# Kernel optimization log

Hardware: AMD Instinct MI355X
Metric: run time of the kernel (lower is better)

## Reference

```python
import jax, jax.numpy as jnp
import numpy as np

B = 32; D = 192; DEPTH = 4; DI = 384; DS = 16; DC = 4; P = 16; IMG = 224; N = 196; NC = 2


def setup_inputs() -> dict:
    key = jax.random.key(0)
    ks = iter(jax.random.split(key, 20))
    rn = lambda shape, s=0.02: jax.random.normal(next(ks), shape, dtype=jnp.float32) * s
    inp = {}
    inp["x"] = jax.random.normal(next(ks), (B, 3, IMG, IMG), dtype=jnp.float32)
    inp["patch_w"] = rn((D, 3 * P * P)); inp["patch_b"] = jnp.zeros((D,), jnp.float32)
    inp["cls_token"] = rn((1, 1, D)); inp["pos_embed"] = rn((1, N + 1, D))
    inp["ln_g"] = jnp.ones((DEPTH, D), jnp.float32); inp["ln_b"] = jnp.zeros((DEPTH, D), jnp.float32)
    inp["w_in"] = rn((DEPTH, 2 * DI, D))
    inp["conv_w"] = rn((DEPTH, DI, DC)); inp["conv_b"] = jnp.zeros((DEPTH, DI), jnp.float32)
    inp["w_x"] = rn((DEPTH, 2 * DS + 1, DI))
    inp["w_dt"] = rn((DEPTH, DI)); inp["b_dt"] = jnp.zeros((DEPTH, DI), jnp.float32)
    A = jnp.tile(jnp.arange(1, DS + 1, dtype=jnp.float32)[None, None, :], (DEPTH, DI, 1))
    inp["A_log"] = jnp.log(A)
    inp["D_ssm"] = jnp.ones((DEPTH, DI), jnp.float32)
    inp["w_out"] = rn((DEPTH, D, DI))
    inp["fn_g"] = jnp.ones((D,), jnp.float32); inp["fn_b"] = jnp.zeros((D,), jnp.float32)
    inp["cls_w"] = rn((NC, D)); inp["cls_b"] = jnp.zeros((NC,), jnp.float32)
    inp["reg_w1"] = rn((D // 2, D)); inp["reg_b1"] = jnp.zeros((D // 2,), jnp.float32)
    inp["reg_w2"] = rn((1, D // 2)); inp["reg_b2"] = jnp.zeros((1,), jnp.float32)
    return inp


def _ln(x, g, b):
    m = x.mean(-1, keepdims=True)
    v = ((x - m) ** 2).mean(-1, keepdims=True)
    return (x - m) / jnp.sqrt(v + 1e-5) * g + b


def _mamba(x, w_in, conv_w, conv_b, w_x, w_dt, b_dt, A_log, D_ssm, w_out):
    Bb, L, _ = x.shape
    xz = jnp.einsum('bld,ed->ble', x, w_in)           # [B,L,2*DI]
    xc, z = xz[..., :DI], xz[..., DI:]
    # causal depthwise conv1d (torch pads both sides then slices [:L] -> left-pad DC-1)
    xct = jnp.transpose(xc, (0, 2, 1))                 # [B,DI,L]
    xpad = jnp.pad(xct, ((0, 0), (0, 0), (DC - 1, 0)))
    conv = sum(conv_w[:, k, None] * xpad[:, :, k:k + L] for k in range(DC)) + conv_b[:, None]
    xa = jax.nn.silu(jnp.transpose(conv, (0, 2, 1)))   # [B,L,DI]
    bcd = jnp.einsum('bld,nd->bln', xa, w_x)           # [B,L,2*DS+1]
    Bm = bcd[..., :DS]; Cm = bcd[..., DS:2 * DS]
    dt = jax.nn.softplus(bcd[..., -1:] * w_dt + b_dt)  # [B,L,DI]  (Linear(1,DI))
    A = -jnp.exp(A_log)                                # [DI,DS]
    dA = jnp.exp(dt[..., None] * A)                    # [B,L,DI,DS]
    dBx = dt[..., None] * Bm[:, :, None, :] * xa[..., None]

    def step(h, inp):
        dA_t, dBx_t, C_t = inp
        h = dA_t * h + dBx_t
        return h, jnp.einsum('bdn,bn->bd', h, C_t)

    h0 = jnp.zeros((Bb, DI, DS), dtype=x.dtype)
    _, ys = jax.lax.scan(step, h0, (dA.transpose(1, 0, 2, 3), dBx.transpose(1, 0, 2, 3), Cm.transpose(1, 0, 2)))
    y = jnp.transpose(ys, (1, 0, 2)) + xa * D_ssm
    return jnp.einsum('bli,di->bld', y * jax.nn.silu(z), w_out)


def reference(x, patch_w, patch_b, cls_token, pos_embed, ln_g, ln_b, w_in, conv_w, conv_b,
              w_x, w_dt, b_dt, A_log, D_ssm, w_out, fn_g, fn_b, cls_w, cls_b,
              reg_w1, reg_b1, reg_w2, reg_b2):
    Bb = x.shape[0]
    H = IMG // P
    # non-overlapping patchify == Conv2d(kernel=stride=P)
    patches = x.reshape(Bb, 3, H, P, H, P).transpose(0, 2, 4, 1, 3, 5).reshape(Bb, N, 3 * P * P)
    tok = patches @ patch_w.T + patch_b
    t = jnp.concatenate([jnp.broadcast_to(cls_token, (Bb, 1, D)), tok], axis=1) + pos_embed
    for i in range(DEPTH):
        t = t + _mamba(_ln(t, ln_g[i], ln_b[i]), w_in[i], conv_w[i], conv_b[i],
                       w_x[i], w_dt[i], b_dt[i], A_log[i], D_ssm[i], w_out[i])
    feat = _ln(t, fn_g, fn_b)[:, 0]
    cls = feat @ cls_w.T + cls_b
    reg = jax.nn.gelu(feat @ reg_w1.T + reg_b1, approximate=False) @ reg_w2.T + reg_b2
    return (cls, reg)
```

## Files before the change

### kernel.cpp

```cpp
#include <hip/hip_runtime.h>
#include <hip/hip_bf16.h>
#include <math.h>

#define B_ 32
#define D_ 192
#define DEPTH_ 4
#define DI_ 384
#define DS_ 16
#define DC_ 4
#define P_ 16
#define IMG_ 224
#define N_ 196
#define L_ 197

#define NCH 16
#define CHL 13

typedef short s16x8 __attribute__((ext_vector_type(8)));
typedef float f32x16 __attribute__((ext_vector_type(16)));

__device__ __forceinline__ float sigmoidf_(float x) { return 1.f / (1.f + expf(-x)); }

__global__ __launch_bounds__(256) void k_prep(const float* __restrict__ patch_w,
                                              const float* __restrict__ w_in,
                                              const float* __restrict__ w_out,
                                              const float* __restrict__ w_x,
                                              const float* __restrict__ cls_tok,
                                              const float* __restrict__ pos,
                                              const float* __restrict__ A_log,
                                              __hip_bfloat16* __restrict__ pw,
                                              __hip_bfloat16* __restrict__ win,
                                              __hip_bfloat16* __restrict__ wout,
                                              __hip_bfloat16* __restrict__ wx,
                                              float* __restrict__ t,
                                              float* __restrict__ Aneg) {
  int idx = blockIdx.x * 256 + threadIdx.x;
  if (idx < 147456) { pw[idx] = __float2bfloat16(patch_w[idx]); return; }
  idx -= 147456;
  if (idx < 589824) { win[idx] = __float2bfloat16(w_in[idx]); return; }
  idx -= 589824;
  if (idx < 294912) { wout[idx] = __float2bfloat16(w_out[idx]); return; }
  idx -= 294912;
  if (idx < 98304) {
    int li = idx / 24576;
    int r = (idx / 384) & 63;
    int c = idx % 384;
    wx[idx] = (r < 33) ? __float2bfloat16(w_x[(li * 33 + r) * 384 + c]) : __float2bfloat16(0.f);
    return;
  }
  idx -= 98304;
  if (idx < 6144) {
    int b = idx / 192, d = idx % 192;
    t[(size_t)b * L_ * D_ + d] = cls_tok[d] + pos[d];
    return;
  }
  idx -= 6144;
  Aneg[idx] = -expf(A_log[idx]);
}

__global__ __launch_bounds__(256) void k_im2col(const float* __restrict__ x,
                                                __hip_bfloat16* __restrict__ A) {
  int idx = blockIdx.x * 256 + threadIdx.x;
  int tok = idx / 768, f = idx - tok * 768;
  int b = tok / 196, p = tok - b * 196;
  int h = p / 14, w = p - h * 14;
  int c = f >> 8, i = (f >> 4) & 15, j = f & 15;
  float v = x[(((size_t)(b * 3 + c) * 224 + h * 16 + i) * 224 + w * 16 + j)];
  A[idx] = __float2bfloat16(v);
}

template <int KTOT, int MODE>
__global__ __launch_bounds__(256) void k_gemm_mfma(const short* __restrict__ A,
                                                   const short* __restrict__ Wb,
                                                   float* __restrict__ C,
                                                   const float* __restrict__ bias,
                                                   const float* __restrict__ pos,
                                                   int M) {
  constexpr int KC = 96;
  constexpr int STR = 104;
  __shared__ __align__(16) short Als[64 * STR];
  __shared__ __align__(16) short Bls[64 * STR];
  int m0 = blockIdx.x * 64, n0 = blockIdx.y * 64;
  int tid = threadIdx.x;
  int lane = tid & 63, wid = tid >> 6;
  int mw = (wid & 1) * 32, nw = (wid >> 1) * 32;
  int l31 = lane & 31, lh = lane >> 5;
  f32x16 acc;
#pragma unroll
  for (int i = 0; i < 16; i++) acc[i] = 0.f;
  for (int kc = 0; kc < KTOT; kc += KC) {
    __syncthreads();
#pragma unroll
    for (int i = 0; i < 3; i++) {
      int seg = tid + i * 256;
      int r = seg / 12, s = seg - r * 12;
      *(s16x8*)(Als + r * STR + s * 8) =
          *(const s16x8*)(A + (size_t)(m0 + r) * KTOT + kc + s * 8);
      *(s16x8*)(Bls + r * STR + s * 8) =
          *(const s16x8*)(Wb + (size_t)(n0 + r) * KTOT + kc + s * 8);
    }
    __syncthreads();
#pragma unroll
    for (int ks = 0; ks < KC / 16; ks++) {
      s16x8 af = *(const s16x8*)(Als + (mw + l31) * STR + ks * 16 + lh * 8);
      s16x8 bf = *(const s16x8*)(Bls + (nw + l31) * STR + ks * 16 + lh * 8);
      acc = __builtin_amdgcn_mfma_f32_32x32x16_bf16(af, bf, acc, 0, 0, 0);
    }
  }
  int gn = n0 + nw + l31;
#pragma unroll
  for (int i = 0; i < 16; i++) {
    int rowt = mw + (i & 3) + 8 * (i >> 2) + 4 * lh;
    int gm = m0 + rowt;
    float v = acc[i];
    if (MODE == 1) {
      if (gm < M) C[(size_t)gm * 192 + gn] += v;
    } else if (MODE == 3) {
      if (gm < M) C[(size_t)gm * 64 + gn] = v;
    } else if (MODE == 4) {
      if (gm < M) ((__hip_bfloat16*)C)[(size_t)gm * 768 + gn] = __float2bfloat16(v);
    } else {
      int b = gm / 196, p = gm - b * 196;
      C[((size_t)b * 197 + 1 + p) * 192 + gn] =
          v + bias[gn] + pos[(size_t)(1 + p) * 192 + gn];
    }
  }
}

__global__ __launch_bounds__(256) void k_ln_bf(const float* __restrict__ t,
                                               const float* __restrict__ g,
                                               const float* __restrict__ bb,
                                               __hip_bfloat16* __restrict__ o) {
  int tok = blockIdx.x * 4 + (threadIdx.x >> 6);
  int tid = threadIdx.x & 63;
  const float* xr = t + (size_t)tok * D_;
  float x0 = xr[tid], x1 = xr[tid + 64], x2 = xr[tid + 128];
  float s = x0 + x1 + x2;
  float q = x0 * x0 + x1 * x1 + x2 * x2;
#pragma unroll
  for (int off = 1; off < 64; off <<= 1) {
    s += __shfl_xor(s, off, 64);
    q += __shfl_xor(q, off, 64);
  }
  float m = s * (1.f / 192.f);
  float r = rsqrtf(q * (1.f / 192.f) - m * m + 1e-5f);
  __hip_bfloat16* orow = o + (size_t)tok * D_;
  orow[tid]       = __float2bfloat16((x0 - m) * r * g[tid]       + bb[tid]);
  orow[tid + 64]  = __float2bfloat16((x1 - m) * r * g[tid + 64]  + bb[tid + 64]);
  orow[tid + 128] = __float2bfloat16((x2 - m) * r * g[tid + 128] + bb[tid + 128]);
}

__global__ __launch_bounds__(384) void k_conv(const __hip_bfloat16* __restrict__ xz,
                                              const float* __restrict__ cw_,
                                              const float* __restrict__ cb,
                                              __hip_bfloat16* __restrict__ xa_bf,
                                              __hip_bfloat16* __restrict__ sz_bf) {
  __shared__ float xs[11][384];
  int r0 = blockIdx.x * 8;
  int d = threadIdx.x;
#pragma unroll
  for (int row = 0; row < 11; row++) {
    int gr = r0 - 3 + row;
    if (gr >= 0) xs[row][d] = __bfloat162float(xz[(size_t)gr * 768 + d]);
  }
  __syncthreads();
  float4 cw = *(const float4*)(cw_ + d * 4);
  float cbv = cb[d];
#pragma unroll
  for (int tk = 0; tk < 8; tk++) {
    int tok = r0 + tk;
    int l = tok % L_;
    float acc = fmaf(cw.w, xs[tk + 3][d], cbv);
    if (l >= 1) acc = fmaf(cw.z, xs[tk + 2][d], acc);
    if (l >= 2) acc = fmaf(cw.y, xs[tk + 1][d], acc);
    if (l >= 3) acc = fmaf(cw.x, xs[tk][d], acc);
    float xav = acc * sigmoidf_(acc);
    xa_bf[(size_t)tok * DI_ + d] = __float2bfloat16(xav);
    float z = __bfloat162float(xz[(size_t)tok * 768 + 384 + d]);
    sz_bf[(size_t)tok * DI_ + d] = __float2bfloat16(z * sigmoidf_(z));
  }
}

__global__ __launch_bounds__(384) void k_scan1(const __hip_bfloat16* __restrict__ xa,
                                               const float* __restrict__ bcd,
                                               const float* __restrict__ Aneg,
                                               const float* __restrict__ w_dt,
                                               const float* __restrict__ b_dt,
                                               float* __restrict__ Pst,
                                               float* __restrict__ Hst) {
  int b = blockIdx.x >> 4, ch = blockIdx.x & 15;
  int d = threadIdx.x;
  int l0 = ch * CHL;
  int lim = min(CHL, L_ - l0);
  float Av[16];
#pragma unroll
  for (int q = 0; q < 4; q++) {
    float4 v = *(const float4*)(Aneg + d * 16 + q * 4);
    Av[q * 4] = v.x; Av[q * 4 + 1] = v.y; Av[q * 4 + 2] = v.z; Av[q * 4 + 3] = v.w;
  }
  float wdt = w_dt[d], bdt = b_dt[d];
  const __hip_bfloat16* xap = xa + ((size_t)b * L_ + l0) * DI_ + d;
  const float* bp = bcd + ((size_t)b * L_ + l0) * 64;
  float h[16], Pp[16];
#pragma unroll
  for (int n = 0; n < 16; n++) { h[n] = 0.f; Pp[n] = 1.f; }
  float xv = __bfloat162float(xap[0]);
  for (int j = 0; j < lim; j++) {
    int jn = (j + 1 < lim) ? (j + 1) : j;
    float xn = __bfloat162float(xap[(size_t)jn * DI_]);
    float dtraw = bp[j * 64 + 32];
    float Bn[16];
#pragma unroll
    for (int n = 0; n < 16; n++) Bn[n] = bp[j * 64 + n];
    float v = fmaf(dtraw, wdt, bdt);
    float dtv = (v > 20.f) ? v : __logf(1.f + __expf(v));
    float dtx = dtv * xv;
#pragma unroll
    for (int n = 0; n < 16; n++) {
      float dA = __expf(dtv * Av[n]);
      h[n] = fmaf(dA, h[n], dtx * Bn[n]);
      Pp[n] *= dA;
    }
    xv = xn;
  }
  size_t s = ((size_t)blockIdx.x * 384 + d) * 16;
#pragma unroll
  for (int q = 0; q < 4; q++) {
    *(float4*)(Pst + s + q * 4) = make_float4(Pp[q * 4], Pp[q * 4 + 1], Pp[q * 4 + 2], Pp[q * 4 + 3]);
    *(float4*)(Hst + s + q * 4) = make_float4(h[q * 4], h[q * 4 + 1], h[q * 4 + 2], h[q * 4 + 3]);
  }
}

__global__ __launch_bounds__(256) void k_scan_mid(const float* __restrict__ Pst,
                                                  const float* __restrict__ Hst,
                                                  float* __restrict__ Hinit) {
  int idx = blockIdx.x * 256 + threadIdx.x;
  int b = idx / 6144, r = idx - b * 6144;
  float h = 0.f;
#pragma unroll
  for (int c = 0; c < NCH; c++) {
    size_t o = (size_t)(b * NCH + c) * 6144 + r;
    Hinit[o] = h;
    h = fmaf(Pst[o], h, Hst[o]);
  }
}

__global__ __launch_bounds__(384) void k_scan2(const __hip_bfloat16* __restrict__ xa,
                                               const __hip_bfloat16* __restrict__ sz,
                                               const float* __restrict__ bcd,
                                               const float* __restrict__ Aneg,
                                               const float* __restrict__ D_ssm,
                                               const float* __restrict__ w_dt,
                                               const float* __restrict__ b_dt,
                                               const float* __restrict__ Hinit,
                                               __hip_bfloat16* __restrict__ y) {
  int b = blockIdx.x >> 4, ch = blockIdx.x & 15;
  int d = threadIdx.x;
  int l0 = ch * CHL;
  int lim = min(CHL, L_ - l0);
  float Av[16];
#pragma unroll
  for (int q = 0; q < 4; q++) {
    float4 v = *(const float4*)(Aneg + d * 16 + q * 4);
    Av[q * 4] = v.x; Av[q * 4 + 1] = v.y; Av[q * 4 + 2] = v.z; Av[q * 4 + 3] = v.w;
  }
  float Dv = D_ssm[d];
  float wdt = w_dt[d], bdt = b_dt[d];
  const __hip_bfloat16* xap = xa + ((size_t)b * L_ + l0) * DI_ + d;
  const __hip_bfloat16* szp = sz + ((size_t)b * L_ + l0) * DI_ + d;
  const float* bp = bcd + ((size_t)b * L_ + l0) * 64;
  __hip_bfloat16* yp = y + ((size_t)b * L_ + l0) * DI_ + d;
  float h[16];
  {
    size_t s = ((size_t)blockIdx.x * 384 + d) * 16;
#pragma unroll
    for (int q = 0; q < 4; q++) {
      float4 v = *(const float4*)(Hinit + s + q * 4);
      h[q * 4] = v.x; h[q * 4 + 1] = v.y; h[q * 4 + 2] = v.z; h[q * 4 + 3] = v.w;
    }
  }
  float xv = __bfloat162float(xap[0]);
  float szv = __bfloat162float(szp[0]);
  for (int j = 0; j < lim; j++) {
    int jn = (j + 1 < lim) ? (j + 1) : j;
    float xn = __bfloat162float(xap[(size_t)jn * DI_]);
    float szn = __bfloat162float(szp[(size_t)jn * DI_]);
    float dtraw = bp[j * 64 + 32];
    float Bn[16], Cn[16];
#pragma unroll
    for (int n = 0; n < 16; n++) Bn[n] = bp[j * 64 + n];
#pragma unroll
    for (int n = 0; n < 16; n++) Cn[n] = bp[j * 64 + 16 + n];
    float v = fmaf(dtraw, wdt, bdt);
    float dtv = (v > 20.f) ? v : __logf(1.f + __expf(v));
    float dtx = dtv * xv;
    float acc = 0.f;
#pragma unroll
    for (int n = 0; n < 16; n++) {
      float dA = __expf(dtv * Av[n]);
      h[n] = fmaf(dA, h[n], dtx * Bn[n]);
      acc = fmaf(h[n], Cn[n], acc);
    }
    float yv = fmaf(xv, Dv, acc) * szv;
    yp[(size_t)j * DI_] = __float2bfloat16(yv);
    xv = xn; szv = szn;
  }
}

__global__ __launch_bounds__(192) void k_head(const float* __restrict__ t,
                                              const float* __restrict__ fn_g,
                                              const float* __restrict__ fn_b,
                                              const float* __restrict__ cls_w,
                                              const float* __restrict__ cls_b,
                                              const float* __restrict__ rw1,
                                              const float* __restrict__ rb1,
                                              const float* __restrict__ rw2,
                                              const float* __restrict__ rb2,
                                              float* __restrict__ out) {
  __shared__ float red[8];
  __shared__ float stats[2];
  __shared__ float feat_s[192];
  __shared__ float h_s[96];
  int b = blockIdx.x, tid = threadIdx.x;
  float x = t[(size_t)b * L_ * D_ + tid];
  float s = x, q = x * x;
#pragma unroll
  for (int off = 1; off < 64; off <<= 1) {
    s += __shfl_xor(s, off, 64);
    q += __shfl_xor(q, off, 64);
  }
  int w = tid >> 6;
  if ((tid & 63) == 0) { red[w] = s; red[4 + w] = q; }
  __syncthreads();
  if (tid == 0) {
    float ss = red[0] + red[1] + red[2];
    float qq = red[4] + red[5] + red[6];
    float m = ss * (1.f / 192.f);
    stats[0] = m;
    stats[1] = rsqrtf(qq * (1.f / 192.f) - m * m + 1e-5f);
  }
  __syncthreads();
  float fv = (x - stats[0]) * stats[1] * fn_g[tid] + fn_b[tid];
  feat_s[tid] = fv;
  __syncthreads();
  if (tid < 96) {
    float a = rb1[tid];
    const float* wr = rw1 + (size_t)tid * 192;
    for (int k = 0; k < 192; k++) a = fmaf(feat_s[k], wr[k], a);
    h_s[tid] = 0.5f * a * (1.f + erff(a * 0.70710678118654752f));
  } else if (tid < 98) {
    int c = tid - 96;
    float a = cls_b[c];
    const float* wr = cls_w + (size_t)c * 192;
    for (int k = 0; k < 192; k++) a = fmaf(feat_s[k], wr[k], a);
    out[b * 2 + c] = a;
  }
  __syncthreads();
  if (tid == 0) {
    float a = rb2[0];
    for (int j = 0; j < 96; j++) a = fmaf(h_s[j], rw2[j], a);
    out[64 + b] = a;
  }
}

extern "C" void kernel_launch(void* const* d_in, const int* in_sizes, int n_in,
                              void* d_out, int out_size, void* d_ws, size_t ws_size,
                              hipStream_t stream) {
  const float* x       = (const float*)d_in[0];
  const float* patch_w = (const float*)d_in[1];
  const float* patch_b = (const float*)d_in[2];
  const float* cls_tok = (const float*)d_in[3];
  const float* pos     = (const float*)d_in[4];
  const float* ln_g    = (const float*)d_in[5];
  const float* ln_b    = (const float*)d_in[6];
  const float* w_in    = (const float*)d_in[7];
  const float* conv_w  = (const float*)d_in[8];
  const float* conv_b  = (const float*)d_in[9];
  const float* w_x     = (const float*)d_in[10];
  const float* w_dt    = (const float*)d_in[11];
  const float* b_dt    = (const float*)d_in[12];
  const float* A_log   = (const float*)d_in[13];
  const float* D_ssm   = (const float*)d_in[14];
  const float* w_out   = (const float*)d_in[15];
  const float* fn_g    = (const float*)d_in[16];
  const float* fn_b    = (const float*)d_in[17];
  const float* cls_w   = (const float*)d_in[18];
  const float* cls_b   = (const float*)d_in[19];
  const float* reg_w1  = (const float*)d_in[20];
  const float* reg_b1  = (const float*)d_in[21];
  const float* reg_w2  = (const float*)d_in[22];
  const float* reg_b2  = (const float*)d_in[23];
  float* out = (float*)d_out;

  float* ws = (float*)d_ws;
  float* t_buf = ws;
  float* bcd   = t_buf + 1210368;
  float* Pst   = bcd + 405504;
  float* Hst   = Pst + 3145728;
  float* Hinit = Hst + 3145728;
  float* Aneg  = Hinit + 3145728;
  __hip_bfloat16* xz_bf  = (__hip_bfloat16*)(Aneg + 24576);
  __hip_bfloat16* Abuf   = xz_bf;
  __hip_bfloat16* xa_bf  = xz_bf + 4841472;
  __hip_bfloat16* sz_bf  = xa_bf + 2433024;
  __hip_bfloat16* xln_bf = sz_bf + 2433024;
  __hip_bfloat16* y_bf   = xln_bf + 1216512;
  __hip_bfloat16* pw_bf  = y_bf + 2433024;
  __hip_bfloat16* win_bf = pw_bf + 147456;
  __hip_bfloat16* wout_bf = win_bf + 589824;
  __hip_bfloat16* wx_bf  = wout_bf + 294912;

  k_prep<<<4536, 256, 0, stream>>>(patch_w, w_in, w_out, w_x, cls_tok, pos, A_log,
                                   pw_bf, win_bf, wout_bf, wx_bf, t_buf, Aneg);
  k_im2col<<<18816, 256, 0, stream>>>(x, Abuf);
  k_gemm_mfma<768, 2><<<dim3(98, 3), 256, 0, stream>>>(
      (const short*)Abuf, (const short*)pw_bf, t_buf, patch_b, pos, 6272);

  for (int i = 0; i < DEPTH_; i++) {
    k_ln_bf<<<1576, 256, 0, stream>>>(t_buf, ln_g + i * D_, ln_b + i * D_, xln_bf);
    k_gemm_mfma<192, 4><<<dim3(99, 12), 256, 0, stream>>>(
        (const short*)xln_bf, (const short*)(win_bf + (size_t)i * 147456), (float*)xz_bf,
        nullptr, nullptr, 6304);
    k_conv<<<788, 384, 0, stream>>>(xz_bf, conv_w + i * DI_ * DC_, conv_b + i * DI_,
                                    xa_bf, sz_bf);
    k_gemm_mfma<384, 3><<<dim3(99, 1), 256, 0, stream>>>(
        (const short*)xa_bf, (const short*)(wx_bf + (size_t)i * 24576), bcd,
        nullptr, nullptr, 6304);
    k_scan1<<<B_ * NCH, 384, 0, stream>>>(xa_bf, bcd, Aneg + i * 6144,
                                          w_dt + i * DI_, b_dt + i * DI_, Pst, Hst);
    k_scan_mid<<<768, 256, 0, stream>>>(Pst, Hst, Hinit);
    k_scan2<<<B_ * NCH, 384, 0, stream>>>(xa_bf, sz_bf, bcd, Aneg + i * 6144,
                                          D_ssm + i * DI_, w_dt + i * DI_, b_dt + i * DI_,
                                          Hinit, y_bf);
    k_gemm_mfma<384, 1><<<dim3(99, 3), 256, 0, stream>>>(
        (const short*)y_bf, (const short*)(wout_bf + (size_t)i * 73728), t_buf,
        nullptr, nullptr, 6304);
  }
  k_head<<<32, 192, 0, stream>>>(t_buf, fn_g, fn_b, cls_w, cls_b, reg_w1, reg_b1,
                                 reg_w2, reg_b2, out);
}
```

Before: 462.0 us.

## Fuse LayerNorm into GEMM epilogues, conv into x_proj GEMM, inline scan combine

Merges im2col with weight prep. The patch GEMM and the out-projection GEMM now use full-row 64x192 tiles, so each can add the residual and compute the next layer's LayerNorm in its epilogue. The depthwise conv plus SiLU now feeds the B/C/dt projection GEMM through shared memory, and the z-gate SiLU is computed in the same kernel. The separate scan_mid kernel is removed: each scan2 block recomputes its chunk-initial state from the per-chunk P/H summaries. This cuts launches and global round-trips, but the full-row GEMMs run only 99 blocks, which lowers parallelism, and later scan chunks repeat the prefix work.

```diff
diff --git a/kernel.cpp b/kernel.cpp
--- a/kernel.cpp
+++ b/kernel.cpp
@@ -20,21 +20,35 @@
 typedef float f32x16 __attribute__((ext_vector_type(16)));
 
 __device__ __forceinline__ float sigmoidf_(float x) { return 1.f / (1.f + expf(-x)); }
-
-__global__ __launch_bounds__(256) void k_prep(const float* __restrict__ patch_w,
-                                              const float* __restrict__ w_in,
-                                              const float* __restrict__ w_out,
-                                              const float* __restrict__ w_x,
-                                              const float* __restrict__ cls_tok,
-                                              const float* __restrict__ pos,
-                                              const float* __restrict__ A_log,
-                                              __hip_bfloat16* __restrict__ pw,
-                                              __hip_bfloat16* __restrict__ win,
-                                              __hip_bfloat16* __restrict__ wout,
-                                              __hip_bfloat16* __restrict__ wx,
-                                              float* __restrict__ t,
-                                              float* __restrict__ Aneg) {
-  int idx = blockIdx.x * 256 + threadIdx.x;
+__device__ __forceinline__ float bf2f(short s) {
+  unsigned int u = ((unsigned int)(unsigned short)s) << 16;
+  return __uint_as_float(u);
+}
+__device__ __forceinline__ short f2bf(float f) {
+  __hip_bfloat16 h = __float2bfloat16(f);
+  return *(short*)&h;
+}
+
+__global__ __launch_bounds__(256) void k_prep_im2col(
+    const float* __restrict__ x, __hip_bfloat16* __restrict__ A,
+    const float* __restrict__ patch_w, const float* __restrict__ w_in,
+    const float* __restrict__ w_out, const float* __restrict__ w_x,
+    const float* __restrict__ cls_tok, const float* __restrict__ pos,
+    const float* __restrict__ A_log,
+    __hip_bfloat16* __restrict__ pw, __hip_bfloat16* __restrict__ win,
+    __hip_bfloat16* __restrict__ wout, __hip_bfloat16* __restrict__ wx,
+    float* __restrict__ t, float* __restrict__ Aneg) {
+  if (blockIdx.x < 18816) {
+    int idx = blockIdx.x * 256 + threadIdx.x;
+    int tok = idx / 768, f = idx - tok * 768;
+    int b = tok / 196, p = tok - b * 196;
+    int h = p / 14, w = p - h * 14;
+    int c = f >> 8, i = (f >> 4) & 15, j = f & 15;
+    float v = x[(((size_t)(b * 3 + c) * 224 + h * 16 + i) * 224 + w * 16 + j)];
+    A[idx] = __float2bfloat16(v);
+    return;
+  }
+  int idx = (blockIdx.x - 18816) * 256 + threadIdx.x;
   if (idx < 147456) { pw[idx] = __float2bfloat16(patch_w[idx]); return; }
   idx -= 147456;
   if (idx < 589824) { win[idx] = __float2bfloat16(w_in[idx]); return; }
@@ -58,25 +72,104 @@
   Aneg[idx] = -expf(A_log[idx]);
 }
 
-__global__ __launch_bounds__(256) void k_im2col(const float* __restrict__ x,
-                                                __hip_bfloat16* __restrict__ A) {
-  int idx = blockIdx.x * 256 + threadIdx.x;
-  int tok = idx / 768, f = idx - tok * 768;
-  int b = tok / 196, p = tok - b * 196;
-  int h = p / 14, w = p - h * 14;
-  int c = f >> 8, i = (f >> 4) & 15, j = f & 15;
-  float v = x[(((size_t)(b * 3 + c) * 224 + h * 16 + i) * 224 + w * 16 + j)];
-  A[idx] = __float2bfloat16(v);
-}
-
-template <int KTOT, int MODE>
-__global__ __launch_bounds__(256) void k_gemm_mfma(const short* __restrict__ A,
-                                                   const short* __restrict__ Wb,
-                                                   float* __restrict__ C,
-                                                   const float* __restrict__ bias,
-                                                   const float* __restrict__ pos,
-                                                   int M) {
-  constexpr int KC = 96;
+__global__ __launch_bounds__(256) void k_patch_ln(const short* __restrict__ A,
+                                                  const short* __restrict__ pw,
+                                                  const float* __restrict__ pb,
+                                                  const float* __restrict__ pos,
+                                                  float* __restrict__ t,
+                                                  const float* __restrict__ g,
+                                                  const float* __restrict__ bb,
+                                                  __hip_bfloat16* __restrict__ xln) {
+  __shared__ __align__(16) char smem[53248];
+  short* Als = (short*)smem;
+  short* Bls = Als + 64 * 104;
+  float* ts = (float*)smem;
+  int m0 = blockIdx.x * 64;
+  int tid = threadIdx.x;
+  int lane = tid & 63, wid = tid >> 6;
+  int mw = (wid & 1) * 32, nw = (wid >> 1) * 96;
+  int l31 = lane & 31, lh = lane >> 5;
+  f32x16 acc[3];
+#pragma unroll
+  for (int j = 0; j < 3; j++)
+#pragma unroll
+    for (int i = 0; i < 16; i++) acc[j][i] = 0.f;
+  for (int kc = 0; kc < 768; kc += 96) {
+    __syncthreads();
+#pragma unroll
+    for (int i = 0; i < 3; i++) {
+      int seg = tid + i * 256;
+      int r = seg / 12, s = seg - r * 12;
+      int tok = m0 + r;
+      int b = tok / 197, l = tok - b * 197;
+      s16x8 v = {0, 0, 0, 0, 0, 0, 0, 0};
+      if (tok < 6304 && l > 0)
+        v = *(const s16x8*)(A + ((size_t)(b * 196 + l - 1)) * 768 + kc + s * 8);
+      *(s16x8*)(Als + r * 104 + s * 8) = v;
+    }
+#pragma unroll
+    for (int i = 0; i < 9; i++) {
+      int seg = tid + i * 256;
+      int r = seg / 12, s = seg - r * 12;
+      *(s16x8*)(Bls + r * 104 + s * 8) = *(const s16x8*)(pw + (size_t)r * 768 + kc + s * 8);
+    }
+    __syncthreads();
+#pragma unroll
+    for (int ks = 0; ks < 6; ks++) {
+      s16x8 af = *(const s16x8*)(Als + (mw + l31) * 104 + ks * 16 + lh * 8);
+#pragma unroll
+      for (int j = 0; j < 3; j++) {
+        s16x8 bf = *(const s16x8*)(Bls + (nw + j * 32 + l31) * 104 + ks * 16 + lh * 8);
+        acc[j] = __builtin_amdgcn_mfma_f32_32x32x16_bf16(af, bf, acc[j], 0, 0, 0);
+      }
+    }
+  }
+  __syncthreads();
+#pragma unroll
+  for (int j = 0; j < 3; j++) {
+    int gnl = nw + j * 32 + l31;
+#pragma unroll
+    for (int i = 0; i < 16; i++) {
+      int rowt = mw + (i & 3) + 8 * (i >> 2) + 4 * lh;
+      ts[rowt * 193 + gnl] = acc[j][i];
+    }
+  }
+  __syncthreads();
+  int r = tid >> 2, part = tid & 3;
+  int tok = m0 + r;
+  int l = tok % 197;
+  bool valid = tok < 6304;
+  float* trow = t + (size_t)tok * 192;
+  float s = 0.f, q = 0.f;
+  for (int jj = 0; jj < 48; jj++) {
+    int col = part * 48 + jj;
+    float v;
+    if (l == 0) {
+      v = valid ? trow[col] : 0.f;
+    } else {
+      v = ts[r * 193 + col] + pb[col] + pos[(size_t)l * 192 + col];
+      if (valid) trow[col] = v;
+    }
+    ts[r * 193 + col] = v;
+    s += v; q += v * v;
+  }
+  s += __shfl_xor(s, 1, 4); s += __shfl_xor(s, 2, 4);
+  q += __shfl_xor(q, 1, 4); q += __shfl_xor(q, 2, 4);
+  float m = s * (1.f / 192.f);
+  float rinv = rsqrtf(q * (1.f / 192.f) - m * m + 1e-5f);
+  if (valid) {
+    __hip_bfloat16* xrow = xln + (size_t)tok * 192;
+    for (int jj = 0; jj < 48; jj++) {
+      int col = part * 48 + jj;
+      float v = ts[r * 193 + col];
+      xrow[col] = __float2bfloat16((v - m) * rinv * g[col] + bb[col]);
+    }
+  }
+}
+
+__global__ __launch_bounds__(256) void k_gemm_in(const short* __restrict__ A,
+                                                 const short* __restrict__ Wb,
+                                                 __hip_bfloat16* __restrict__ C) {
   constexpr int STR = 104;
   __shared__ __align__(16) short Als[64 * STR];
   __shared__ __align__(16) short Bls[64 * STR];
@@ -88,20 +181,20 @@
   f32x16 acc;
 #pragma unroll
   for (int i = 0; i < 16; i++) acc[i] = 0.f;
-  for (int kc = 0; kc < KTOT; kc += KC) {
+  for (int kc = 0; kc < 192; kc += 96) {
     __syncthreads();
 #pragma unroll
     for (int i = 0; i < 3; i++) {
       int seg = tid + i * 256;
       int r = seg / 12, s = seg - r * 12;
       *(s16x8*)(Als + r * STR + s * 8) =
-          *(const s16x8*)(A + (size_t)(m0 + r) * KTOT + kc + s * 8);
+          *(const s16x8*)(A + (size_t)(m0 + r) * 192 + kc + s * 8);
       *(s16x8*)(Bls + r * STR + s * 8) =
-          *(const s16x8*)(Wb + (size_t)(n0 + r) * KTOT + kc + s * 8);
-    }
-    __syncthreads();
-#pragma unroll
-    for (int ks = 0; ks < KC / 16; ks++) {
+          *(const s16x8*)(Wb + (size_t)(n0 + r) * 192 + kc + s * 8);
+    }
+    __syncthreads();
+#pragma unroll
+    for (int ks = 0; ks < 6; ks++) {
       s16x8 af = *(const s16x8*)(Als + (mw + l31) * STR + ks * 16 + lh * 8);
       s16x8 bf = *(const s16x8*)(Bls + (nw + l31) * STR + ks * 16 + lh * 8);
       acc = __builtin_amdgcn_mfma_f32_32x32x16_bf16(af, bf, acc, 0, 0, 0);
@@ -112,72 +205,104 @@
   for (int i = 0; i < 16; i++) {
     int rowt = mw + (i & 3) + 8 * (i >> 2) + 4 * lh;
     int gm = m0 + rowt;
-    float v = acc[i];
-    if (MODE == 1) {
-      if (gm < M) C[(size_t)gm * 192 + gn] += v;
-    } else if (MODE == 3) {
-      if (gm < M) C[(size_t)gm * 64 + gn] = v;
-    } else if (MODE == 4) {
-      if (gm < M) ((__hip_bfloat16*)C)[(size_t)gm * 768 + gn] = __float2bfloat16(v);
-    } else {
-      int b = gm / 196, p = gm - b * 196;
-      C[((size_t)b * 197 + 1 + p) * 192 + gn] =
-          v + bias[gn] + pos[(size_t)(1 + p) * 192 + gn];
-    }
-  }
-}
-
-__global__ __launch_bounds__(256) void k_ln_bf(const float* __restrict__ t,
-                                               const float* __restrict__ g,
-                                               const float* __restrict__ bb,
-                                               __hip_bfloat16* __restrict__ o) {
-  int tok = blockIdx.x * 4 + (threadIdx.x >> 6);
-  int tid = threadIdx.x & 63;
-  const float* xr = t + (size_t)tok * D_;
-  float x0 = xr[tid], x1 = xr[tid + 64], x2 = xr[tid + 128];
-  float s = x0 + x1 + x2;
-  float q = x0 * x0 + x1 * x1 + x2 * x2;
-#pragma unroll
-  for (int off = 1; off < 64; off <<= 1) {
-    s += __shfl_xor(s, off, 64);
-    q += __shfl_xor(q, off, 64);
-  }
-  float m = s * (1.f / 192.f);
-  float r = rsqrtf(q * (1.f / 192.f) - m * m + 1e-5f);
-  __hip_bfloat16* orow = o + (size_t)tok * D_;
-  orow[tid]       = __float2bfloat16((x0 - m) * r * g[tid]       + bb[tid]);
-  orow[tid + 64]  = __float2bfloat16((x1 - m) * r * g[tid + 64]  + bb[tid + 64]);
-  orow[tid + 128] = __float2bfloat16((x2 - m) * r * g[tid + 128] + bb[tid + 128]);
-}
-
-__global__ __launch_bounds__(384) void k_conv(const __hip_bfloat16* __restrict__ xz,
-                                              const float* __restrict__ cw_,
-                                              const float* __restrict__ cb,
-                                              __hip_bfloat16* __restrict__ xa_bf,
-                                              __hip_bfloat16* __restrict__ sz_bf) {
-  __shared__ float xs[11][384];
-  int r0 = blockIdx.x * 8;
-  int d = threadIdx.x;
-#pragma unroll
-  for (int row = 0; row < 11; row++) {
-    int gr = r0 - 3 + row;
-    if (gr >= 0) xs[row][d] = __bfloat162float(xz[(size_t)gr * 768 + d]);
-  }
-  __syncthreads();
-  float4 cw = *(const float4*)(cw_ + d * 4);
-  float cbv = cb[d];
-#pragma unroll
-  for (int tk = 0; tk < 8; tk++) {
-    int tok = r0 + tk;
-    int l = tok % L_;
-    float acc = fmaf(cw.w, xs[tk + 3][d], cbv);
-    if (l >= 1) acc = fmaf(cw.z, xs[tk + 2][d], acc);
-    if (l >= 2) acc = fmaf(cw.y, xs[tk + 1][d], acc);
-    if (l >= 3) acc = fmaf(cw.x, xs[tk][d], acc);
-    float xav = acc * sigmoidf_(acc);
-    xa_bf[(size_t)tok * DI_ + d] = __float2bfloat16(xav);
-    float z = __bfloat162float(xz[(size_t)tok * 768 + 384 + d]);
-    sz_bf[(size_t)tok * DI_ + d] = __float2bfloat16(z * sigmoidf_(z));
+    if (gm < 6304) C[(size_t)gm * 768 + gn] = __float2bfloat16(acc[i]);
+  }
+}
+
+__global__ __launch_bounds__(256) void k_convbcd(const __hip_bfloat16* __restrict__ xz,
+                                                 const float* __restrict__ cw_,
+                                                 const float* __restrict__ cb_,
+                                                 const short* __restrict__ wx,
+                                                 float* __restrict__ bcd,
+                                                 __hip_bfloat16* __restrict__ xa_bf,
+                                                 __hip_bfloat16* __restrict__ sz_bf) {
+  __shared__ float xs[67 * 96];
+  __shared__ __align__(16) short Als[64 * 104];
+  __shared__ __align__(16) short Bls[64 * 104];
+  __shared__ float cws[96 * 4];
+  __shared__ float cbs[96];
+  int m0 = blockIdx.x * 64;
+  int tid = threadIdx.x;
+  int lane = tid & 63, wid = tid >> 6;
+  int mw = (wid & 1) * 32, nw = (wid >> 1) * 32;
+  int l31 = lane & 31, lh = lane >> 5;
+  f32x16 acc;
+#pragma unroll
+  for (int i = 0; i < 16; i++) acc[i] = 0.f;
+  for (int kc = 0; kc < 384; kc += 96) {
+    __syncthreads();
+#pragma unroll
+    for (int i = 0; i < 4; i++) {
+      int seg = tid + i * 256;
+      if (seg < 804) {
+        int row = seg / 12, s = seg - row * 12;
+        int tokp = m0 - 3 + row;
+        s16x8 v = {0, 0, 0, 0, 0, 0, 0, 0};
+        if (tokp >= 0 && tokp < 6304)
+          v = *(const s16x8*)((const short*)xz + (size_t)tokp * 768 + kc + s * 8);
+        float4 f0 = make_float4(bf2f(v[0]), bf2f(v[1]), bf2f(v[2]), bf2f(v[3]));
+        float4 f1 = make_float4(bf2f(v[4]), bf2f(v[5]), bf2f(v[6]), bf2f(v[7]));
+        *(float4*)(xs + row * 96 + s * 8) = f0;
+        *(float4*)(xs + row * 96 + s * 8 + 4) = f1;
+      }
+    }
+    if (tid < 96) {
+      *(float4*)(cws + tid * 4) = *(const float4*)(cw_ + (kc + tid) * 4);
+      cbs[tid] = cb_[kc + tid];
+    }
+#pragma unroll
+    for (int i = 0; i < 3; i++) {
+      int seg = tid + i * 256;
+      int r = seg / 12, s = seg - r * 12;
+      *(s16x8*)(Bls + r * 104 + s * 8) = *(const s16x8*)(wx + (size_t)r * 384 + kc + s * 8);
+    }
+    __syncthreads();
+#pragma unroll
+    for (int i = 0; i < 24; i++) {
+      int idx = tid + i * 256;
+      int orow = idx / 96, c = idx - orow * 96;
+      int tok = m0 + orow;
+      int l = tok % 197;
+      float4 cw = *(const float4*)(cws + c * 4);
+      float a = fmaf(cw.w, xs[(orow + 3) * 96 + c], cbs[c]);
+      if (l >= 1) a = fmaf(cw.z, xs[(orow + 2) * 96 + c], a);
+      if (l >= 2) a = fmaf(cw.y, xs[(orow + 1) * 96 + c], a);
+      if (l >= 3) a = fmaf(cw.x, xs[orow * 96 + c], a);
+      float xav = a * sigmoidf_(a);
+      short bv = f2bf(xav);
+      Als[orow * 104 + c] = bv;
+      if (tok < 6304) ((short*)xa_bf)[(size_t)tok * 384 + kc + c] = bv;
+    }
+    __syncthreads();
+#pragma unroll
+    for (int ks = 0; ks < 6; ks++) {
+      s16x8 af = *(const s16x8*)(Als + (mw + l31) * 104 + ks * 16 + lh * 8);
+      s16x8 bf = *(const s16x8*)(Bls + (nw + l31) * 104 + ks * 16 + lh * 8);
+      acc = __builtin_amdgcn_mfma_f32_32x32x16_bf16(af, bf, acc, 0, 0, 0);
+    }
+  }
+  int gn = nw + l31;
+#pragma unroll
+  for (int i = 0; i < 16; i++) {
+    int rowt = mw + (i & 3) + 8 * (i >> 2) + 4 * lh;
+    int gm = m0 + rowt;
+    if (gm < 6304) bcd[(size_t)gm * 64 + gn] = acc[i];
+  }
+#pragma unroll
+  for (int i = 0; i < 12; i++) {
+    int seg = tid + i * 256;
+    int r = seg / 48, s = seg - r * 48;
+    int tok = m0 + r;
+    if (tok < 6304) {
+      s16x8 zv = *(const s16x8*)((const short*)xz + (size_t)tok * 768 + 384 + s * 8);
+      s16x8 ov;
+#pragma unroll
+      for (int e = 0; e < 8; e++) {
+        float z = bf2f(zv[e]);
+        ov[e] = f2bf(z * sigmoidf_(z));
+      }
+      *(s16x8*)((short*)sz_bf + (size_t)tok * 384 + s * 8) = ov;
+    }
   }
 }
 
@@ -231,20 +356,6 @@
   }
 }
 
-__global__ __launch_bounds__(256) void k_scan_mid(const float* __restrict__ Pst,
-                                                  const float* __restrict__ Hst,
-                                                  float* __restrict__ Hinit) {
-  int idx = blockIdx.x * 256 + threadIdx.x;
-  int b = idx / 6144, r = idx - b * 6144;
-  float h = 0.f;
-#pragma unroll
-  for (int c = 0; c < NCH; c++) {
-    size_t o = (size_t)(b * NCH + c) * 6144 + r;
-    Hinit[o] = h;
-    h = fmaf(Pst[o], h, Hst[o]);
-  }
-}
-
 __global__ __launch_bounds__(384) void k_scan2(const __hip_bfloat16* __restrict__ xa,
                                                const __hip_bfloat16* __restrict__ sz,
                                                const float* __restrict__ bcd,
@@ -252,7 +363,8 @@
                                                const float* __restrict__ D_ssm,
                                                const float* __restrict__ w_dt,
                                                const float* __restrict__ b_dt,
-                                               const float* __restrict__ Hinit,
+                                               const float* __restrict__ Pst,
+                                               const float* __restrict__ Hst,
                                                __hip_bfloat16* __restrict__ y) {
   int b = blockIdx.x >> 4, ch = blockIdx.x & 15;
   int d = threadIdx.x;
@@ -266,19 +378,25 @@
   }
   float Dv = D_ssm[d];
   float wdt = w_dt[d], bdt = b_dt[d];
+  float h[16];
+#pragma unroll
+  for (int n = 0; n < 16; n++) h[n] = 0.f;
+  for (int c = 0; c < ch; c++) {
+    size_t o = ((size_t)(b * NCH + c) * 384 + d) * 16;
+#pragma unroll
+    for (int q = 0; q < 4; q++) {
+      float4 P = *(const float4*)(Pst + o + q * 4);
+      float4 H = *(const float4*)(Hst + o + q * 4);
+      h[q * 4]     = fmaf(P.x, h[q * 4],     H.x);
+      h[q * 4 + 1] = fmaf(P.y, h[q * 4 + 1], H.y);
+      h[q * 4 + 2] = fmaf(P.z, h[q * 4 + 2], H.z);
+      h[q * 4 + 3] = fmaf(P.w, h[q * 4 + 3], H.w);
+    }
+  }
   const __hip_bfloat16* xap = xa + ((size_t)b * L_ + l0) * DI_ + d;
   const __hip_bfloat16* szp = sz + ((size_t)b * L_ + l0) * DI_ + d;
   const float* bp = bcd + ((size_t)b * L_ + l0) * 64;
   __hip_bfloat16* yp = y + ((size_t)b * L_ + l0) * DI_ + d;
-  float h[16];
-  {
-    size_t s = ((size_t)blockIdx.x * 384 + d) * 16;
-#pragma unroll
-    for (int q = 0; q < 4; q++) {
-      float4 v = *(const float4*)(Hinit + s + q * 4);
-      h[q * 4] = v.x; h[q * 4 + 1] = v.y; h[q * 4 + 2] = v.z; h[q * 4 + 3] = v.w;
-    }
-  }
   float xv = __bfloat162float(xap[0]);
   float szv = __bfloat162float(szp[0]);
   for (int j = 0; j < lim; j++) {
@@ -304,6 +422,95 @@
     float yv = fmaf(xv, Dv, acc) * szv;
     yp[(size_t)j * DI_] = __float2bfloat16(yv);
     xv = xn; szv = szn;
+  }
+}
+
+template <bool DO_LN>
+__global__ __launch_bounds__(256) void k_out_ln(const short* __restrict__ A,
+                                                const short* __restrict__ wout,
+                                                float* __restrict__ t,
+                                                const float* __restrict__ g,
+                                                const float* __restrict__ bb,
+                                                __hip_bfloat16* __restrict__ xln) {
+  __shared__ __align__(16) char smem[53248];
+  short* Als = (short*)smem;
+  short* Bls = Als + 64 * 104;
+  float* ts = (float*)smem;
+  int m0 = blockIdx.x * 64;
+  int tid = threadIdx.x;
+  int lane = tid & 63, wid = tid >> 6;
+  int mw = (wid & 1) * 32, nw = (wid >> 1) * 96;
+  int l31 = lane & 31, lh = lane >> 5;
+  f32x16 acc[3];
+#pragma unroll
+  for (int j = 0; j < 3; j++)
+#pragma unroll
+    for (int i = 0; i < 16; i++) acc[j][i] = 0.f;
+  for (int kc = 0; kc < 384; kc += 96) {
+    __syncthreads();
+#pragma unroll
+    for (int i = 0; i < 3; i++) {
+      int seg = tid + i * 256;
+      int r = seg / 12, s = seg - r * 12;
+      *(s16x8*)(Als + r * 104 + s * 8) =
+          *(const s16x8*)(A + (size_t)(m0 + r) * 384 + kc + s * 8);
+    }
+#pragma unroll
+    for (int i = 0; i < 9; i++) {
+      int seg = tid + i * 256;
+      int r = seg / 12, s = seg - r * 12;
+      *(s16x8*)(Bls + r * 104 + s * 8) = *(const s16x8*)(wout + (size_t)r * 384 + kc + s * 8);
+    }
+    __syncthreads();
+#pragma unroll
+    for (int ks = 0; ks < 6; ks++) {
+      s16x8 af = *(const s16x8*)(Als + (mw + l31) * 104 + ks * 16 + lh * 8);
+#pragma unroll
+      for (int j = 0; j < 3; j++) {
+        s16x8 bf = *(const s16x8*)(Bls + (nw + j * 32 + l31) * 104 + ks * 16 + lh * 8);
+        acc[j] = __builtin_amdgcn_mfma_f32_32x32x16_bf16(af, bf, acc[j], 0, 0, 0);
+      }
+    }
+  }
+  __syncthreads();
+#pragma unroll
+  for (int j = 0; j < 3; j++) {
+    int gnl = nw + j * 32 + l31;
+#pragma unroll
+    for (int i = 0; i < 16; i++) {
+      int rowt = mw + (i & 3) + 8 * (i >> 2) + 4 * lh;
+      ts[rowt * 193 + gnl] = acc[j][i];
+    }
+  }
+  __syncthreads();
+  int r = tid >> 2, part = tid & 3;
+  int tok = m0 + r;
+  bool valid = tok < 6304;
+  float* trow = t + (size_t)tok * 192;
+  float s = 0.f, q = 0.f;
+  for (int jj = 0; jj < 48; jj++) {
+    int col = part * 48 + jj;
+    float v = ts[r * 193 + col];
+    if (valid) {
+      v += trow[col];
+      trow[col] = v;
+    }
+    ts[r * 193 + col] = v;
+    s += v; q += v * v;
+  }
+  if (DO_LN) {
+    s += __shfl_xor(s, 1, 4); s += __shfl_xor(s, 2, 4);
+    q += __shfl_xor(q, 1, 4); q += __shfl_xor(q, 2, 4);
+    float m = s * (1.f / 192.f);
+    float rinv = rsqrtf(q * (1.f / 192.f) - m * m + 1e-5f);
+    if (valid) {
+      __hip_bfloat16* xrow = xln + (size_t)tok * 192;
+      for (int jj = 0; jj < 48; jj++) {
+        int col = part * 48 + jj;
+        float v = ts[r * 193 + col];
+        xrow[col] = __float2bfloat16((v - m) * rinv * g[col] + bb[col]);
+      }
+    }
   }
 }
 
@@ -397,8 +604,7 @@
   float* bcd   = t_buf + 1210368;
   float* Pst   = bcd + 405504;
   float* Hst   = Pst + 3145728;
-  float* Hinit = Hst + 3145728;
-  float* Aneg  = Hinit + 3145728;
+  float* Aneg  = Hst + 3145728;
   __hip_bfloat16* xz_bf  = (__hip_bfloat16*)(Aneg + 24576);
   __hip_bfloat16* Abuf   = xz_bf;
   __hip_bfloat16* xa_bf  = xz_bf + 4841472;
@@ -410,31 +616,32 @@
   __hip_bfloat16* wout_bf = win_bf + 589824;
   __hip_bfloat16* wx_bf  = wout_bf + 294912;
 
-  k_prep<<<4536, 256, 0, stream>>>(patch_w, w_in, w_out, w_x, cls_tok, pos, A_log,
-                                   pw_bf, win_bf, wout_bf, wx_bf, t_buf, Aneg);
-  k_im2col<<<18816, 256, 0, stream>>>(x, Abuf);
-  k_gemm_mfma<768, 2><<<dim3(98, 3), 256, 0, stream>>>(
-      (const short*)Abuf, (const short*)pw_bf, t_buf, patch_b, pos, 6272);
+  k_prep_im2col<<<23352, 256, 0, stream>>>(x, Abuf, patch_w, w_in, w_out, w_x,
+                                           cls_tok, pos, A_log, pw_bf, win_bf,
+                                           wout_bf, wx_bf, t_buf, Aneg);
+  k_patch_ln<<<99, 256, 0, stream>>>((const short*)Abuf, (const short*)pw_bf,
+                                     patch_b, pos, t_buf, ln_g, ln_b, xln_bf);
 
   for (int i = 0; i < DEPTH_; i++) {
-    k_ln_bf<<<1576, 256, 0, stream>>>(t_buf, ln_g + i * D_, ln_b + i * D_, xln_bf);
-    k_gemm_mfma<192, 4><<<dim3(99, 12), 256, 0, stream>>>(
-        (const short*)xln_bf, (const short*)(win_bf + (size_t)i * 147456), (float*)xz_bf,
-        nullptr, nullptr, 6304);
-    k_conv<<<788, 384, 0, stream>>>(xz_bf, conv_w + i * DI_ * DC_, conv_b + i * DI_,
-                                    xa_bf, sz_bf);
-    k_gemm_mfma<384, 3><<<dim3(99, 1), 256, 0, stream>>>(
-        (const short*)xa_bf, (const short*)(wx_bf + (size_t)i * 24576), bcd,
-        nullptr, nullptr, 6304);
+    k_gemm_in<<<dim3(99, 12), 256, 0, stream>>>(
+        (const short*)xln_bf, (const short*)(win_bf + (size_t)i * 147456), xz_bf);
+    k_convbcd<<<99, 256, 0, stream>>>(xz_bf, conv_w + i * DI_ * DC_, conv_b + i * DI_,
+                                      (const short*)(wx_bf + (size_t)i * 24576),
+                                      bcd, xa_bf, sz_bf);
     k_scan1<<<B_ * NCH, 384, 0, stream>>>(xa_bf, bcd, Aneg + i * 6144,
                                           w_dt + i * DI_, b_dt + i * DI_, Pst, Hst);
-    k_scan_mid<<<768, 256, 0, stream>>>(Pst, Hst, Hinit);
     k_scan2<<<B_ * NCH, 384, 0, stream>>>(xa_bf, sz_bf, bcd, Aneg + i * 6144,
                                           D_ssm + i * DI_, w_dt + i * DI_, b_dt + i * DI_,
-                                          Hinit, y_bf);
-    k_gemm_mfma<384, 1><<<dim3(99, 3), 256, 0, stream>>>(
-        (const short*)y_bf, (const short*)(wout_bf + (size_t)i * 73728), t_buf,
-        nullptr, nullptr, 6304);
+                                          Pst, Hst, y_bf);
+    if (i < DEPTH_ - 1) {
+      k_out_ln<true><<<99, 256, 0, stream>>>(
+          (const short*)y_bf, (const short*)(wout_bf + (size_t)i * 73728), t_buf,
+          ln_g + (i + 1) * D_, ln_b + (i + 1) * D_, xln_bf);
+    } else {
+      k_out_ln<false><<<99, 256, 0, stream>>>(
+          (const short*)y_bf, (const short*)(wout_bf + (size_t)i * 73728), t_buf,
+          nullptr, nullptr, nullptr);
+    }
   }
   k_head<<<32, 192, 0, stream>>>(t_buf, fn_g, fn_b, cls_w, cls_b, reg_w1, reg_b1,
                                  reg_w2, reg_b2, out);
```

Result: slower. 780.5 us (+68.9%).
